# Optimization experiments

Hardware: AMD Instinct MI355X
Metric: run time of the kernel (lower is better)

## Reference

```python
import jax, jax.numpy as jnp
import numpy as np

NUM_CHANS = 64
LAG = 5
HIDDEN = [32, 32]  # module appends a final 1-channel layer
BATCH = 16
T = 2048


def setup_inputs() -> dict:
    key = jax.random.key(0)
    ks = jax.random.split(key, 7)
    p, h0, h1 = NUM_CHANS, HIDDEN[0], HIDDEN[1]
    # Per-network weights stacked along leading axis n = num_series = p.
    # Xavier-ish scale for layer 0 (Conv1d(p, h0, lag)), default-ish for rest.
    s0 = float(np.sqrt(2.0 / (p * LAG + h0)))
    return {
        "X": jax.random.normal(ks[0], (BATCH, T, p), dtype=jnp.float32),
        "W0": jax.random.normal(ks[1], (p, h0, p, LAG), dtype=jnp.float32) * s0,
        "b0": jax.random.normal(ks[2], (p, h0), dtype=jnp.float32) * 0.01,
        "W1": jax.random.normal(ks[3], (p, h1, h0), dtype=jnp.float32) * float(np.sqrt(1.0 / h0)),
        "b1": jax.random.normal(ks[4], (p, h1), dtype=jnp.float32) * 0.01,
        "W2": jax.random.normal(ks[5], (p, 1, h1), dtype=jnp.float32) * float(np.sqrt(1.0 / h1)),
        "b2": jax.random.normal(ks[6], (p, 1), dtype=jnp.float32) * 0.01,
    }


def reference(X, W0, b0, W1, b1, W2, b2):
    # X: [B, T, p]. Each of n=p networks: Conv1d(p,h0,lag) -> ReLU -> Conv1d(h0,h1,1)
    # -> ReLU -> Conv1d(h1,1,1); outputs concatenated along last dim.
    lag = W0.shape[-1]
    Tout = X.shape[1] - lag + 1  # valid conv output length
    # Sliding windows: Xwin[b,t,c,l] = X[b, t+l, c]  -> [B, Tout, p, lag]
    Xwin = jnp.stack([X[:, l:l + Tout, :] for l in range(lag)], axis=-1)
    # Layer 0 across all n networks at once: [B, n, Tout, h0]
    h = jnp.einsum('btcl,nhcl->bnth', Xwin, W0) + b0[None, :, None, :]
    # 1x1 conv layers (per-network dense along channel dim)
    h = jax.nn.relu(h)
    h = jnp.einsum('bnti,noi->bnto', h, W1) + b1[None, :, None, :]
    h = jax.nn.relu(h)
    h = jnp.einsum('bnti,noi->bnto', h, W2) + b2[None, :, None, :]  # [B, n, Tout, 1]
    # concat along dim 2 of (batch, Tout, 1) per network -> (B, Tout, n)
    return jnp.transpose(h[..., 0], (0, 2, 1))
```

## Files before the change

kernel.cpp:

```cpp
#include <hip/hip_runtime.h>

#define NCH 64
#define LAG 5
#define H0 32
#define H1 32
#define TIN 2048
#define TOUT 2044
#define NBATCH 16

#define XSTRIDE 72

typedef __attribute__((ext_vector_type(8))) short short8;
typedef __attribute__((ext_vector_type(4))) short short4v;
typedef __attribute__((ext_vector_type(4))) float f32x4;

__device__ __forceinline__ unsigned short f2bf(float f) {
    unsigned u = __float_as_uint(f);
    u += 0x7fffu + ((u >> 16) & 1u);
    return (unsigned short)(u >> 16);
}

__device__ __forceinline__ unsigned pack2bf_relu(float a, float b) {
    unsigned ua = __float_as_uint(fmaxf(a, 0.0f)) + 0x8000u;
    unsigned ub = __float_as_uint(fmaxf(b, 0.0f)) + 0x8000u;
    return __builtin_amdgcn_perm(ub, ua, 0x07060302u);
}

__device__ __forceinline__ short4v pack4bf_relu(const f32x4& v) {
    union { short4v s; unsigned u[2]; } cv;
    cv.u[0] = pack2bf_relu(v[0], v[1]);
    cv.u[1] = pack2bf_relu(v[2], v[3]);
    return cv.s;
}

__global__ __launch_bounds__(256) void prep_all(
    const float* __restrict__ X,  unsigned short* __restrict__ Xpad,
    const float* __restrict__ W0, unsigned short* __restrict__ W0b,
    const float* __restrict__ W1, unsigned short* __restrict__ W1b,
    const float* __restrict__ W2, unsigned short* __restrict__ W2b)
{
    const int bx = blockIdx.x;
    if (bx < 2048) {
        int j = bx * 256 + threadIdx.x;
        int row = j >> 4, seg = j & 15;
        float4 x = *(const float4*)(X + (size_t)j * 4);
        unsigned long long v = (unsigned long long)f2bf(x.x)
                             | ((unsigned long long)f2bf(x.y) << 16)
                             | ((unsigned long long)f2bf(x.z) << 32)
                             | ((unsigned long long)f2bf(x.w) << 48);
        *(unsigned long long*)(Xpad + (size_t)row * XSTRIDE + seg * 4) = v;
    } else if (bx < 2560) {
        int j = (bx - 2048) * 256 + threadIdx.x;
        int nh = j >> 6, c = j & 63;
        const float* src = W0 + (size_t)j * LAG;
        unsigned short* dst = W0b + nh * 320 + c;
        #pragma unroll
        for (int l = 0; l < LAG; ++l) dst[l * 64] = f2bf(src[l]);
    } else if (bx < 2592) {
        int i = ((bx - 2560) * 256 + threadIdx.x) * 8;
        float4 a = *(const float4*)(W1 + i);
        float4 b = *(const float4*)(W1 + i + 4);
        unsigned long long v0 = (unsigned long long)f2bf(a.x)
                              | ((unsigned long long)f2bf(a.y) << 16)
                              | ((unsigned long long)f2bf(a.z) << 32)
                              | ((unsigned long long)f2bf(a.w) << 48);
        unsigned long long v1 = (unsigned long long)f2bf(b.x)
                              | ((unsigned long long)f2bf(b.y) << 16)
                              | ((unsigned long long)f2bf(b.z) << 32)
                              | ((unsigned long long)f2bf(b.w) << 48);
        *(unsigned long long*)(W1b + i)     = v0;
        *(unsigned long long*)(W1b + i + 4) = v1;
    } else {
        int i = threadIdx.x * 8;
        float4 a = *(const float4*)(W2 + i);
        float4 b = *(const float4*)(W2 + i + 4);
        unsigned long long v0 = (unsigned long long)f2bf(a.x)
                              | ((unsigned long long)f2bf(a.y) << 16)
                              | ((unsigned long long)f2bf(a.z) << 32)
                              | ((unsigned long long)f2bf(a.w) << 48);
        unsigned long long v1 = (unsigned long long)f2bf(b.x)
                              | ((unsigned long long)f2bf(b.y) << 16)
                              | ((unsigned long long)f2bf(b.z) << 32)
                              | ((unsigned long long)f2bf(b.w) << 48);
        *(unsigned long long*)(W2b + i)     = v0;
        *(unsigned long long*)(W2b + i + 4) = v1;
    }
}

__global__ __launch_bounds__(256, 2) void mlp_mfma(
    const unsigned short* __restrict__ Xpad,
    const unsigned short* __restrict__ W0b,
    const unsigned short* __restrict__ W1b,
    const unsigned short* __restrict__ W2b,
    const float* __restrict__ b0, const float* __restrict__ b1,
    const float* __restrict__ b2, float* __restrict__ out)
{
    __shared__ __align__(16) unsigned short xs[37 * 512];
    __shared__ __align__(16) unsigned short yt[256][8];

    const int tileid = blockIdx.x;
    const int ng     = blockIdx.y;
    const int b      = tileid >> 3;
    const int t0     = (tileid & 7) * 256;
    const int tid    = threadIdx.x;
    const int wave   = tid >> 6;
    const int lane   = tid & 63;
    const int quad   = lane >> 4;
    const int l15    = lane & 15;

    {
        const char* srcb = (const char*)(Xpad + (size_t)(b * TIN + t0) * XSTRIDE);
        #pragma unroll 1
        for (int i = wave; i < 37; i += 4) {
            __builtin_amdgcn_global_load_lds(
                (const __attribute__((address_space(1))) unsigned int*)(srcb + i * 1024 + lane * 16),
                (__attribute__((address_space(3))) unsigned int*)((char*)xs + i * 1024),
                16, 0, 0);
        }
    }

    short8 B0[2][10][2];
    short4v A1[2][2][2];
    short4v A2[2][2];
    f32x4 b0q[2][2], b1q[2][2];
    float b2s[2];
    #pragma unroll
    for (int net = 0; net < 2; ++net) {
        const int n = ng * 8 + net * 4 + wave;
        const unsigned short* wp0 = W0b + (n * H0 + l15) * (NCH * LAG) + quad * 8;
        #pragma unroll
        for (int ks = 0; ks < 10; ++ks) {
            B0[net][ks][0] = *(const short8*)(wp0 + ks * 32);
            B0[net][ks][1] = *(const short8*)(wp0 + 16 * (NCH * LAG) + ks * 32);
        }
        #pragma unroll
        for (int of = 0; of < 2; ++of)
            #pragma unroll
            for (int kf = 0; kf < 2; ++kf)
                A1[net][of][kf] = *(const short4v*)(W1b + (n * H1 + of * 16 + l15) * H0 + kf * 16 + quad * 4);
        #pragma unroll
        for (int kf = 0; kf < 2; ++kf)
            A2[net][kf] = *(const short4v*)(W2b + n * H1 + kf * 16 + quad * 4);
        #pragma unroll
        for (int nf = 0; nf < 2; ++nf) b0q[net][nf] = *(const f32x4*)(b0 + (size_t)n * H0 + nf * 16 + quad * 4);
        #pragma unroll
        for (int of = 0; of < 2; ++of) b1q[net][of] = *(const f32x4*)(b1 + (size_t)n * H1 + of * 16 + quad * 4);
        b2s[net] = b2[n];
    }

    __syncthreads();

    const int vmax = (t0 == 1792) ? 251 : 255;

    #pragma unroll 1
    for (int chunk = 0; chunk < 8; ++chunk) {
        #pragma unroll
        for (int mf = 0; mf < 2; ++mf) {
            const int irow = chunk * 32 + mf * 16 + l15;
            const int ic   = irow < vmax ? irow : vmax;
            const int rowoff = ic * XSTRIDE + quad * 8;

            f32x4 acc[2][2];
            #pragma unroll
            for (int net = 0; net < 2; ++net) {
                acc[net][0] = b0q[net][0];
                acc[net][1] = b0q[net][1];
            }
            __builtin_amdgcn_s_setprio(1);
            #pragma unroll
            for (int ks = 0; ks < 10; ++ks) {
                const int xoff = (ks >> 1) * XSTRIDE + (ks & 1) * 32;
                short8 Xf = *(const short8*)&xs[rowoff + xoff];
                acc[0][0] = __builtin_amdgcn_mfma_f32_16x16x32_bf16(B0[0][ks][0], Xf, acc[0][0], 0, 0, 0);
                acc[0][1] = __builtin_amdgcn_mfma_f32_16x16x32_bf16(B0[0][ks][1], Xf, acc[0][1], 0, 0, 0);
                acc[1][0] = __builtin_amdgcn_mfma_f32_16x16x32_bf16(B0[1][ks][0], Xf, acc[1][0], 0, 0, 0);
                acc[1][1] = __builtin_amdgcn_mfma_f32_16x16x32_bf16(B0[1][ks][1], Xf, acc[1][1], 0, 0, 0);
            }
            __builtin_amdgcn_s_setprio(0);

            #pragma unroll
            for (int net = 0; net < 2; ++net) {
                short4v Bh0 = pack4bf_relu(acc[net][0]);
                short4v Bh1 = pack4bf_relu(acc[net][1]);

                f32x4 D1[2] = { b1q[net][0], b1q[net][1] };
                D1[0] = __builtin_amdgcn_mfma_f32_16x16x16bf16_1k(A1[net][0][0], Bh0, D1[0], 0, 0, 0);
                D1[0] = __builtin_amdgcn_mfma_f32_16x16x16bf16_1k(A1[net][0][1], Bh1, D1[0], 0, 0, 0);
                D1[1] = __builtin_amdgcn_mfma_f32_16x16x16bf16_1k(A1[net][1][0], Bh0, D1[1], 0, 0, 0);
                D1[1] = __builtin_amdgcn_mfma_f32_16x16x16bf16_1k(A1[net][1][1], Bh1, D1[1], 0, 0, 0);

                short4v Bg0 = pack4bf_relu(D1[0]);
                short4v Bg1 = pack4bf_relu(D1[1]);

                f32x4 D2 = (f32x4){ b2s[net], b2s[net], b2s[net], b2s[net] };
                D2 = __builtin_amdgcn_mfma_f32_16x16x16bf16_1k(A2[net][0], Bg0, D2, 0, 0, 0);
                D2 = __builtin_amdgcn_mfma_f32_16x16x16bf16_1k(A2[net][1], Bg1, D2, 0, 0, 0);

                if (quad == 0)
                    yt[irow][wave + net * 4] = f2bf(D2[0]);
            }
        }
    }
    __syncthreads();

    int t = t0 + tid;
    if (t < TOUT) {
        short8 v = *(const short8*)yt[tid];
        float4 o0, o1;
        o0.x = __uint_as_float((unsigned)(unsigned short)v[0] << 16);
        o0.y = __uint_as_float((unsigned)(unsigned short)v[1] << 16);
        o0.z = __uint_as_float((unsigned)(unsigned short)v[2] << 16);
        o0.w = __uint_as_float((unsigned)(unsigned short)v[3] << 16);
        o1.x = __uint_as_float((unsigned)(unsigned short)v[4] << 16);
        o1.y = __uint_as_float((unsigned)(unsigned short)v[5] << 16);
        o1.z = __uint_as_float((unsigned)(unsigned short)v[6] << 16);
        o1.w = __uint_as_float((unsigned)(unsigned short)v[7] << 16);
        size_t base = ((size_t)(b * TOUT + t)) * NCH + ng * 8;
        *(float4*)&out[base]     = o0;
        *(float4*)&out[base + 4] = o1;
    }
}

extern "C" void kernel_launch(void* const* d_in, const int* in_sizes, int n_in,
                              void* d_out, int out_size, void* d_ws, size_t ws_size,
                              hipStream_t stream)
{
    const float* X  = (const float*)d_in[0];
    const float* W0 = (const float*)d_in[1];
    const float* b0 = (const float*)d_in[2];
    const float* W1 = (const float*)d_in[3];
    const float* b1 = (const float*)d_in[4];
    const float* W2 = (const float*)d_in[5];
    const float* b2 = (const float*)d_in[6];
    float* out = (float*)d_out;

    unsigned short* Xpad = (unsigned short*)d_ws;
    unsigned short* W0b  = (unsigned short*)((char*)d_ws + 4726784);
    unsigned short* W1b  = (unsigned short*)((char*)d_ws + 6037504);
    unsigned short* W2b  = (unsigned short*)((char*)d_ws + 6168576);

    prep_all<<<2593, 256, 0, stream>>>(X, Xpad, W0, W0b, W1, W1b, W2, W2b);
    mlp_mfma<<<dim3(128, 8), 256, 0, stream>>>(Xpad, W0b, W1b, W2b, b0, b1, b2, out);
}
```

Baseline: 124.8 us.

## Split each block's work across time halves, 4 networks per block

Each block now handles 4 networks instead of 8, and its four waves are arranged as 2 network pairs by 2 time halves, so each wave processes 8 chunks of 16 rows instead of 8 chunks of 32 rows. The grid doubles to 128x16 blocks, which halves per-block work and raises parallelism and occupancy across CUs. In exchange, the X tile is loaded into LDS twice as often in total, and the output stores shrink to 16 bytes per row.

```diff
diff --git a/kernel.cpp b/kernel.cpp
--- a/kernel.cpp
+++ b/kernel.cpp
@@ -96,7 +96,7 @@
     const float* __restrict__ b2, float* __restrict__ out)
 {
     __shared__ __align__(16) unsigned short xs[37 * 512];
-    __shared__ __align__(16) unsigned short yt[256][8];
+    __shared__ __align__(8)  unsigned short yt[256][4];
 
     const int tileid = blockIdx.x;
     const int ng     = blockIdx.y;
@@ -107,6 +107,8 @@
     const int lane   = tid & 63;
     const int quad   = lane >> 4;
     const int l15    = lane & 15;
+    const int ph     = wave >> 1;
+    const int nh     = wave & 1;
 
     {
         const char* srcb = (const char*)(Xpad + (size_t)(b * TIN + t0) * XSTRIDE);
@@ -126,7 +128,7 @@
     float b2s[2];
     #pragma unroll
     for (int net = 0; net < 2; ++net) {
-        const int n = ng * 8 + net * 4 + wave;
+        const int n = ng * 4 + nh * 2 + net;
         const unsigned short* wp0 = W0b + (n * H0 + l15) * (NCH * LAG) + quad * 8;
         #pragma unroll
         for (int ks = 0; ks < 10; ++ks) {
@@ -142,9 +144,9 @@
         for (int kf = 0; kf < 2; ++kf)
             A2[net][kf] = *(const short4v*)(W2b + n * H1 + kf * 16 + quad * 4);
         #pragma unroll
-        for (int nf = 0; nf < 2; ++nf) b0q[net][nf] = *(const f32x4*)(b0 + (size_t)n * H0 + nf * 16 + quad * 4);
-        #pragma unroll
-        for (int of = 0; of < 2; ++of) b1q[net][of] = *(const f32x4*)(b1 + (size_t)n * H1 + of * 16 + quad * 4);
+        for (int f = 0; f < 2; ++f) b0q[net][f] = *(const f32x4*)(b0 + (size_t)n * H0 + f * 16 + quad * 4);
+        #pragma unroll
+        for (int f = 0; f < 2; ++f) b1q[net][f] = *(const f32x4*)(b1 + (size_t)n * H1 + f * 16 + quad * 4);
         b2s[net] = b2[n];
     }
 
@@ -154,70 +156,61 @@
 
     #pragma unroll 1
     for (int chunk = 0; chunk < 8; ++chunk) {
-        #pragma unroll
-        for (int mf = 0; mf < 2; ++mf) {
-            const int irow = chunk * 32 + mf * 16 + l15;
-            const int ic   = irow < vmax ? irow : vmax;
-            const int rowoff = ic * XSTRIDE + quad * 8;
-
-            f32x4 acc[2][2];
-            #pragma unroll
-            for (int net = 0; net < 2; ++net) {
-                acc[net][0] = b0q[net][0];
-                acc[net][1] = b0q[net][1];
-            }
-            __builtin_amdgcn_s_setprio(1);
-            #pragma unroll
-            for (int ks = 0; ks < 10; ++ks) {
-                const int xoff = (ks >> 1) * XSTRIDE + (ks & 1) * 32;
-                short8 Xf = *(const short8*)&xs[rowoff + xoff];
-                acc[0][0] = __builtin_amdgcn_mfma_f32_16x16x32_bf16(B0[0][ks][0], Xf, acc[0][0], 0, 0, 0);
-                acc[0][1] = __builtin_amdgcn_mfma_f32_16x16x32_bf16(B0[0][ks][1], Xf, acc[0][1], 0, 0, 0);
-                acc[1][0] = __builtin_amdgcn_mfma_f32_16x16x32_bf16(B0[1][ks][0], Xf, acc[1][0], 0, 0, 0);
-                acc[1][1] = __builtin_amdgcn_mfma_f32_16x16x32_bf16(B0[1][ks][1], Xf, acc[1][1], 0, 0, 0);
-            }
-            __builtin_amdgcn_s_setprio(0);
-
-            #pragma unroll
-            for (int net = 0; net < 2; ++net) {
-                short4v Bh0 = pack4bf_relu(acc[net][0]);
-                short4v Bh1 = pack4bf_relu(acc[net][1]);
-
-                f32x4 D1[2] = { b1q[net][0], b1q[net][1] };
-                D1[0] = __builtin_amdgcn_mfma_f32_16x16x16bf16_1k(A1[net][0][0], Bh0, D1[0], 0, 0, 0);
-                D1[0] = __builtin_amdgcn_mfma_f32_16x16x16bf16_1k(A1[net][0][1], Bh1, D1[0], 0, 0, 0);
-                D1[1] = __builtin_amdgcn_mfma_f32_16x16x16bf16_1k(A1[net][1][0], Bh0, D1[1], 0, 0, 0);
-                D1[1] = __builtin_amdgcn_mfma_f32_16x16x16bf16_1k(A1[net][1][1], Bh1, D1[1], 0, 0, 0);
-
-                short4v Bg0 = pack4bf_relu(D1[0]);
-                short4v Bg1 = pack4bf_relu(D1[1]);
-
-                f32x4 D2 = (f32x4){ b2s[net], b2s[net], b2s[net], b2s[net] };
-                D2 = __builtin_amdgcn_mfma_f32_16x16x16bf16_1k(A2[net][0], Bg0, D2, 0, 0, 0);
-                D2 = __builtin_amdgcn_mfma_f32_16x16x16bf16_1k(A2[net][1], Bg1, D2, 0, 0, 0);
-
-                if (quad == 0)
-                    yt[irow][wave + net * 4] = f2bf(D2[0]);
-            }
+        const int irow = ph * 128 + chunk * 16 + l15;
+        const int ic   = irow < vmax ? irow : vmax;
+        const int rowoff = ic * XSTRIDE + quad * 8;
+
+        f32x4 acc[2][2];
+        #pragma unroll
+        for (int net = 0; net < 2; ++net) {
+            acc[net][0] = b0q[net][0];
+            acc[net][1] = b0q[net][1];
+        }
+        __builtin_amdgcn_s_setprio(1);
+        #pragma unroll
+        for (int ks = 0; ks < 10; ++ks) {
+            const int xoff = (ks >> 1) * XSTRIDE + (ks & 1) * 32;
+            short8 Xf = *(const short8*)&xs[rowoff + xoff];
+            acc[0][0] = __builtin_amdgcn_mfma_f32_16x16x32_bf16(B0[0][ks][0], Xf, acc[0][0], 0, 0, 0);
+            acc[0][1] = __builtin_amdgcn_mfma_f32_16x16x32_bf16(B0[0][ks][1], Xf, acc[0][1], 0, 0, 0);
+            acc[1][0] = __builtin_amdgcn_mfma_f32_16x16x32_bf16(B0[1][ks][0], Xf, acc[1][0], 0, 0, 0);
+            acc[1][1] = __builtin_amdgcn_mfma_f32_16x16x32_bf16(B0[1][ks][1], Xf, acc[1][1], 0, 0, 0);
+        }
+        __builtin_amdgcn_s_setprio(0);
+
+        #pragma unroll
+        for (int net = 0; net < 2; ++net) {
+            short4v Bh0 = pack4bf_relu(acc[net][0]);
+            short4v Bh1 = pack4bf_relu(acc[net][1]);
+
+            f32x4 D1[2] = { b1q[net][0], b1q[net][1] };
+            D1[0] = __builtin_amdgcn_mfma_f32_16x16x16bf16_1k(A1[net][0][0], Bh0, D1[0], 0, 0, 0);
+            D1[0] = __builtin_amdgcn_mfma_f32_16x16x16bf16_1k(A1[net][0][1], Bh1, D1[0], 0, 0, 0);
+            D1[1] = __builtin_amdgcn_mfma_f32_16x16x16bf16_1k(A1[net][1][0], Bh0, D1[1], 0, 0, 0);
+            D1[1] = __builtin_amdgcn_mfma_f32_16x16x16bf16_1k(A1[net][1][1], Bh1, D1[1], 0, 0, 0);
+
+            short4v Bg0 = pack4bf_relu(D1[0]);
+            short4v Bg1 = pack4bf_relu(D1[1]);
+
+            f32x4 D2 = (f32x4){ b2s[net], b2s[net], b2s[net], b2s[net] };
+            D2 = __builtin_amdgcn_mfma_f32_16x16x16bf16_1k(A2[net][0], Bg0, D2, 0, 0, 0);
+            D2 = __builtin_amdgcn_mfma_f32_16x16x16bf16_1k(A2[net][1], Bg1, D2, 0, 0, 0);
+
+            if (quad == 0)
+                yt[ph * 128 + chunk * 16 + l15][nh * 2 + net] = f2bf(D2[0]);
         }
     }
     __syncthreads();
 
     int t = t0 + tid;
     if (t < TOUT) {
-        short8 v = *(const short8*)yt[tid];
-        float4 o0, o1;
-        o0.x = __uint_as_float((unsigned)(unsigned short)v[0] << 16);
-        o0.y = __uint_as_float((unsigned)(unsigned short)v[1] << 16);
-        o0.z = __uint_as_float((unsigned)(unsigned short)v[2] << 16);
-        o0.w = __uint_as_float((unsigned)(unsigned short)v[3] << 16);
-        o1.x = __uint_as_float((unsigned)(unsigned short)v[4] << 16);
-        o1.y = __uint_as_float((unsigned)(unsigned short)v[5] << 16);
-        o1.z = __uint_as_float((unsigned)(unsigned short)v[6] << 16);
-        o1.w = __uint_as_float((unsigned)(unsigned short)v[7] << 16);
-        size_t base = ((size_t)(b * TOUT + t)) * NCH + ng * 8;
-        *(float4*)&out[base]     = o0;
-        *(float4*)&out[base + 4] = o1;
+        ushort4 v = *(const ushort4*)yt[tid];
+        float4 o;
+        o.x = __uint_as_float((unsigned)v.x << 16);
+        o.y = __uint_as_float((unsigned)v.y << 16);
+        o.z = __uint_as_float((unsigned)v.z << 16);
+        o.w = __uint_as_float((unsigned)v.w << 16);
+        *(float4*)&out[((size_t)(b * TOUT + t)) * NCH + ng * 4] = o;
     }
 }
 
@@ -240,5 +233,5 @@
     unsigned short* W2b  = (unsigned short*)((char*)d_ws + 6168576);
 
     prep_all<<<2593, 256, 0, stream>>>(X, Xpad, W0, W0b, W1, W1b, W2, W2b);
-    mlp_mfma<<<dim3(128, 8), 256, 0, stream>>>(Xpad, W0b, W1b, W2b, b0, b1, b2, out);
-}
+    mlp_mfma<<<dim3(128, 16), 256, 0, stream>>>(Xpad, W0b, W1b, W2b, b0, b1, b2, out);
+}
```

After: 135.6 us. 1.09x slower.
